# Kernel optimization log

Hardware: AMD Instinct MI355X
Metric: run time of the kernel (lower is better)

Reference implementation:

```python
import jax, jax.numpy as jnp
import numpy as np

B, D_IN, FD = 32768, 2048, 128
N1 = N2 = N3 = 4
T = 1.0  # temperature buffer value (eval mode)
LN_EPS = 1e-5

def _gelu(x):
    return jax.nn.gelu(x, approximate=False)  # torch nn.GELU default = exact erf

def setup_inputs() -> dict:
    key = jax.random.key(0)
    ks = iter(jax.random.split(key, 64))
    def rn(shape, s=0.02):
        return jax.random.normal(next(ks), shape, jnp.float32) * s
    inp = {"x": jax.random.normal(next(ks), (B, D_IN), jnp.float32)}
    # input_proj: Linear(2048,512) GELU Linear(512,256) LayerNorm(256)
    inp.update(ipW1=rn((D_IN, 512)), ipb1=jnp.zeros(512), ipW2=rn((512, 256)), ipb2=jnp.zeros(256),
               ln_g=jnp.ones(256), ln_b=jnp.zeros(256))
    def level(din, nc, pfx):
        return {pfx+"W3d": rn((din, 3)), pfx+"b3d": jnp.zeros(3),
                pfx+"c": rn((nc, 3), 0.3), pfx+"lr": jnp.zeros(nc),
                pfx+"f1W": rn((din, FD)), pfx+"f1b": jnp.zeros(FD),
                pfx+"f2W": rn((FD, FD)), pfx+"f2b": jnp.zeros(FD),
                pfx+"rW": rn((FD+3, nc)), pfx+"rb": jnp.zeros(nc)}
    inp.update(level(256, N1, "l1"))
    inp.update(level(FD, N2, "l2"))
    inp.update(level(FD, N3, "l3"))
    # expert_head: Linear(128+4+4+4, 256) GELU Linear(256, 64)
    inp.update(ehW1=rn((FD+N1+N2+N3, 256)), ehb1=jnp.zeros(256),
               ehW2=rn((256, N1*N2*N3)), ehb2=jnp.zeros(N1*N2*N3))
    return inp

def _level_fwd(x, W3d, b3d, c, f1W, f1b, f2W, f2b, rW, rb):
    # x: (B, din) -> probs (B, nc), features (B, FD)
    pos = x @ W3d + b3d                                   # (B, 3)
    d_sq = ((pos[:, None, :] - c[None, :, :]) ** 2).sum(-1)  # (B, nc)
    geo = -d_sq / (2.0 * T * T + 1e-8)                    # non-spectral geo signal
    feat = _gelu(x @ f1W + f1b) @ f2W + f2b               # (B, FD)
    logits = jnp.concatenate([feat, pos], axis=-1) @ rW + rb + 0.5 * geo
    probs = jax.nn.softmax(logits / max(T, 0.1), axis=-1)  # eval path: plain softmax
    return probs, feat

def _router_fwd(x, ipW1, ipb1, ipW2, ipb2, ln_g, ln_b,
                l1W3d, l1b3d, l1c, l1f1W, l1f1b, l1f2W, l1f2b, l1rW, l1rb,
                l2W3d, l2b3d, l2c, l2f1W, l2f1b, l2f2W, l2f2b, l2rW, l2rb,
                l3W3d, l3b3d, l3c, l3f1W, l3f1b, l3f2W, l3f2b, l3rW, l3rb,
                ehW1, ehb1, ehW2, ehb2):
    h = _gelu(x @ ipW1 + ipb1) @ ipW2 + ipb2
    mu = h.mean(-1, keepdims=True)
    var = ((h - mu) ** 2).mean(-1, keepdims=True)
    h = (h - mu) * jax.lax.rsqrt(var + LN_EPS) * ln_g + ln_b  # LayerNorm(256)
    p1, f1 = _level_fwd(h,  l1W3d, l1b3d, l1c, l1f1W, l1f1b, l1f2W, l1f2b, l1rW, l1rb)
    p2, f2 = _level_fwd(f1, l2W3d, l2b3d, l2c, l2f1W, l2f1b, l2f2W, l2f2b, l2rW, l2rb)
    p3, f3 = _level_fwd(f2, l3W3d, l3b3d, l3c, l3f1W, l3f1b, l3f2W, l3f2b, l3rW, l3rb)
    combined = jnp.concatenate([f3, p1, p2, p3], axis=-1)  # (B, 140)
    logits = _gelu(combined @ ehW1 + ehb1) @ ehW2 + ehb2   # (B, 64)
    expert_probs = jax.nn.softmax(logits / max(T, 0.1), axis=-1)
    return expert_probs

def reference(x, ipW1, ipb1, ipW2, ipb2, ln_g, ln_b,
              l1W3d, l1b3d, l1c, l1lr, l1f1W, l1f1b, l1f2W, l1f2b, l1rW, l1rb,
              l2W3d, l2b3d, l2c, l2lr, l2f1W, l2f1b, l2f2W, l2f2b, l2rW, l2rb,
              l3W3d, l3b3d, l3c, l3lr, l3f1W, l3f1b, l3f2W, l3f2b, l3rW, l3rb,
              ehW1, ehb1, ehW2, ehb2):
    # l?lr (log_radii) are unused in non-spectral mode, matching the source.
    expert_probs = _router_fwd(x, ipW1, ipb1, ipW2, ipb2, ln_g, ln_b,
                               l1W3d, l1b3d, l1c, l1f1W, l1f1b, l1f2W, l1f2b, l1rW, l1rb,
                               l2W3d, l2b3d, l2c, l2f1W, l2f1b, l2f2W, l2f2b, l2rW, l2rb,
                               l3W3d, l3b3d, l3c, l3f1W, l3f1b, l3f2W, l3f2b, l3rW, l3rb,
                               ehW1, ehb1, ehW2, ehb2)
    expert_ids = jnp.argmax(expert_probs, axis=-1)
    return expert_probs, expert_ids
```

## Files before the change

### kernel.cpp

```cpp
#include <hip/hip_runtime.h>
#include <hip/hip_bf16.h>
#include <cstdint>
#include <cstddef>


typedef short  s8v  __attribute__((ext_vector_type(8)));
typedef float  f4v  __attribute__((ext_vector_type(4)));
typedef float  f16v __attribute__((ext_vector_type(16)));
typedef unsigned int u32;

#define B_ROWS 32768

__device__ inline short f2bf(float x) {
    __hip_bfloat16 h = __float2bfloat16(x);
    return __builtin_bit_cast(short, h);
}
__device__ inline float bf2f(short s) {
    return __bfloat162float(__builtin_bit_cast(__hip_bfloat16, s));
}
__device__ inline float gelu_f(float x) {
    return 0.5f * x * (1.0f + erff(x * 0.70710678118654752440f));
}
__device__ inline void gload_lds16(const short* g, short* l) {
    __builtin_amdgcn_global_load_lds(
        (const __attribute__((address_space(1))) u32*)g,
        (__attribute__((address_space(3))) u32*)l, 16, 0, 0);
}

__global__ void split_w1_img(const float* __restrict__ W, short* __restrict__ img)
{
    const int idx = blockIdx.x * 256 + threadIdx.x;
    const int p = idx & 7;
    const int n = (idx >> 3) & 511;
    const int t = idx >> 12;
    const int cs = p ^ (n & 7);
    const int plane = cs >> 2, kc = cs & 3;
    const int kbase = t * 32 + kc * 8;
    s8v v8;
    #pragma unroll
    for (int e = 0; e < 8; ++e) {
        const float v = W[(size_t)(kbase + e) * 512 + n];
        const short h = f2bf(v);
        v8[e] = plane ? f2bf(v - bf2f(h)) : h;
    }
    *(s8v*)&img[(size_t)((t * 512 + n) * 64 + p * 8)] = v8;
}

__launch_bounds__(256, 3)
__global__ void gemm1k(const float* __restrict__ X,
                       const short* __restrict__ Bimg,
                       const float* __restrict__ bias,
                       float* __restrict__ out)
{
    __shared__ short smem[128 * 64 * 3];
    short* Ab  = smem;
    short* Bb0 = smem + 128 * 64;
    short* Bb1 = smem + 128 * 64 * 2;

    const int tid = threadIdx.x;
    const int l = tid & 63, wid = tid >> 6;
    const int wr = wid >> 1, wc = wid & 1;

    const int d = blockIdx.x;
    const int xcd = d & 7, s = d >> 3;
    const int m0 = (xcd * 32 + (s >> 2)) * 128;
    const int n0 = (s & 3) * 128;

    const int ar = tid & 127, ah = tid >> 7;
    const float* xP = X + (size_t)(m0 + ar) * 2048 + ah * 16;
    short* awr = Ab + ar * 64;
    const int pw0 = ((ah * 2    ) ^ (ar & 7)) * 8;
    const int pw1 = ((ah * 2 + 1) ^ (ar & 7)) * 8;
    const int pw2 = ((ah * 2 + 4) ^ (ar & 7)) * 8;
    const int pw3 = ((ah * 2 + 5) ^ (ar & 7)) * 8;

    const short* bP = Bimg + (size_t)n0 * 64 + (size_t)(wid * 4) * 512 + (size_t)l * 8;
    const int bdo = wid * 4 * 512;

    f16v acc[2][2];
    #pragma unroll
    for (int m = 0; m < 2; ++m)
        #pragma unroll
        for (int n = 0; n < 2; ++n) acc[m][n] = (f16v)0.0f;

    f4v cur0, cur1, cur2, cur3;

    auto stageB = [&](int t, short* base) {
        const short* bt = bP + (size_t)t * 32768;
        short* bD = base + bdo;
        gload_lds16(bt,        bD);
        gload_lds16(bt +  512, bD + 512);
        gload_lds16(bt + 1024, bD + 1024);
        gload_lds16(bt + 1536, bD + 1536);
    };
    auto loadA = [&](int t) {
        const float* p = xP + t * 32;
        cur0 = *(const f4v*)(p + 0);
        cur1 = *(const f4v*)(p + 4);
        cur2 = *(const f4v*)(p + 8);
        cur3 = *(const f4v*)(p + 12);
    };
    auto compute = [&](const short* Bb) {
        #pragma unroll
        for (int ks = 0; ks < 2; ++ks) {
            const int ph0 = ks * 2 + (l >> 5);
            s8v ahf[2], alf[2], bhf[2], blf[2];
            #pragma unroll
            for (int m = 0; m < 2; ++m) {
                const int row = wr * 64 + m * 32 + (l & 31);
                const int ph = ph0 ^ (row & 7);
                ahf[m] = *(const s8v*)&Ab[row * 64 + ph * 8];
                alf[m] = *(const s8v*)&Ab[row * 64 + (ph ^ 4) * 8];
            }
            #pragma unroll
            for (int n = 0; n < 2; ++n) {
                const int col = wc * 64 + n * 32 + (l & 31);
                const int ph = ph0 ^ (col & 7);
                bhf[n] = *(const s8v*)&Bb[col * 64 + ph * 8];
                blf[n] = *(const s8v*)&Bb[col * 64 + (ph ^ 4) * 8];
            }
            __builtin_amdgcn_s_setprio(1);
            #pragma unroll
            for (int m = 0; m < 2; ++m)
                #pragma unroll
                for (int n = 0; n < 2; ++n) {
                    acc[m][n] = __builtin_amdgcn_mfma_f32_32x32x16_bf16(ahf[m], bhf[n], acc[m][n], 0, 0, 0);
                    acc[m][n] = __builtin_amdgcn_mfma_f32_32x32x16_bf16(ahf[m], blf[n], acc[m][n], 0, 0, 0);
                    acc[m][n] = __builtin_amdgcn_mfma_f32_32x32x16_bf16(alf[m], bhf[n], acc[m][n], 0, 0, 0);
                }
            __builtin_amdgcn_s_setprio(0);
        }
    };
    auto step = [&](int t, short* bcur, short* bnext) {
        s8v hi0, hi1, lo0, lo1;
        #pragma unroll
        for (int e = 0; e < 4; ++e) {
            float v; short h;
            v = cur0[e]; h = f2bf(v); hi0[e]     = h; lo0[e]     = f2bf(v - bf2f(h));
            v = cur1[e]; h = f2bf(v); hi0[e + 4] = h; lo0[e + 4] = f2bf(v - bf2f(h));
            v = cur2[e]; h = f2bf(v); hi1[e]     = h; lo1[e]     = f2bf(v - bf2f(h));
            v = cur3[e]; h = f2bf(v); hi1[e + 4] = h; lo1[e + 4] = f2bf(v - bf2f(h));
        }
        __builtin_amdgcn_s_barrier();
        __builtin_amdgcn_sched_barrier(0);
        *(s8v*)&awr[pw0] = hi0;
        *(s8v*)&awr[pw1] = hi1;
        *(s8v*)&awr[pw2] = lo0;
        *(s8v*)&awr[pw3] = lo1;
        if (t < 63) {
            stageB(t + 1, bnext);
            __builtin_amdgcn_sched_barrier(0);
            loadA(t + 1);
        }
        asm volatile("s_waitcnt lgkmcnt(0)" ::: "memory");
        __builtin_amdgcn_s_barrier();
        __builtin_amdgcn_sched_barrier(0);
        compute(bcur);
    };

    stageB(0, Bb0);
    __builtin_amdgcn_sched_barrier(0);
    loadA(0);
    for (int t = 0; t < 64; t += 2) {
        step(t,     Bb0, Bb1);
        step(t + 1, Bb1, Bb0);
    }

    #pragma unroll
    for (int m = 0; m < 2; ++m) {
        #pragma unroll
        for (int n = 0; n < 2; ++n) {
            const int gcol = n0 + wc * 64 + n * 32 + (l & 31);
            const float bv = bias[gcol];
            #pragma unroll
            for (int r = 0; r < 16; ++r) {
                const int grow = m0 + wr * 64 + m * 32
                               + (r & 3) + 8 * (r >> 2) + 4 * (l >> 5);
                out[(size_t)grow * 512 + gcol] = gelu_f(acc[m][n][r] + bv);
            }
        }
    }
}

struct SplitDesc { const float* W; short* dst; int K, N, Kpad, blk0; };
struct SplitPack { SplitDesc d[9]; };

__global__ void split_all(SplitPack p) {
    const int bid = blockIdx.x;
    int i = 0;
    #pragma unroll
    for (int j = 1; j < 9; ++j) if (bid >= p.d[j].blk0) i = j;
    const SplitDesc& D = p.d[i];
    const int idx = (bid - D.blk0) * 256 + threadIdx.x;
    const int total = D.N * D.Kpad;
    if (idx >= total) return;
    const int n = idx / D.Kpad, k = idx - n * D.Kpad;
    const float v = (k < D.K) ? D.W[(size_t)k * D.N + n] : 0.0f;
    const short hs = f2bf(v);
    D.dst[idx] = hs;
    D.dst[total + idx] = f2bf(v - bf2f(hs));
}

template<int BM, int BN, int EPI>
__launch_bounds__(256, 2)
__global__ void gemm32(const float* __restrict__ A, int lda,
                       const short* __restrict__ Bsp, int ldb, int NK,
                       const float* __restrict__ bias, int K, int N, int ntiles,
                       int ostr, float* __restrict__ out, float* __restrict__ out2)
{
    constexpr int MF  = BM / 64;
    constexpr int NFw = BN / 64;
    constexpr int BUF = (BM + BN) * 64;
    constexpr int FPT = BM / 8;
    constexpr int TPR = 32 / FPT;
    constexpr int nBI = BN / 32;
    __shared__ short smem[2 * BUF];

    const int tid = threadIdx.x;
    const int l   = tid & 63, wid = tid >> 6;
    const int wr  = wid >> 1, wc = wid & 1;
    const int bid = blockIdx.x;
    const int ntb = bid % ntiles, mtb = bid / ntiles;
    const int m0  = mtb * BM, n0 = ntb * BN;

    const int ar = tid / TPR, aseg = tid % TPR;
    const float* aP = A + (size_t)(m0 + ar) * lda + aseg * FPT;

    const short* bg[nBI];
    {
        const int cs = (l & 7) ^ (l >> 3);
        const int plane = cs >> 2, kslot = cs & 3;
        #pragma unroll
        for (int j = 0; j < nBI; ++j) {
            const int col = (wid * nBI + j) * 8 + (l >> 3);
            bg[j] = Bsp + (size_t)plane * NK + (size_t)(n0 + col) * ldb + kslot * 8;
        }
    }

    f16v acc[MF][NFw];
    #pragma unroll
    for (int m = 0; m < MF; ++m)
        #pragma unroll
        for (int n = 0; n < NFw; ++n) acc[m][n] = (f16v)0.0f;

    f4v areg[FPT / 4];

    auto loadA = [&](int t) {
        const float* p = aP + t * 32;
        #pragma unroll
        for (int i = 0; i < FPT / 4; ++i) areg[i] = *(const f4v*)(p + i * 4);
    };
    auto stageB = [&](int t, short* buf) {
        short* Bb = buf + BM * 64;
        #pragma unroll
        for (int j = 0; j < nBI; ++j)
            gload_lds16(bg[j] + t * 32, Bb + (wid * nBI + j) * 512);
    };
    auto writeA = [&](short* buf) {
        #pragma unroll
        for (int c = 0; c < FPT / 8; ++c) {
            s8v hi, lo;
            #pragma unroll
            for (int e = 0; e < 8; ++e) {
                const float v = areg[c * 2 + (e >> 2)][e & 3];
                const short hs = f2bf(v);
                hi[e] = hs; lo[e] = f2bf(v - bf2f(hs));
            }
            const int csh = aseg * (FPT / 8) + c;
            *(s8v*)&buf[ar * 64 + ((csh    ) ^ (ar & 7)) * 8] = hi;
            *(s8v*)&buf[ar * 64 + ((csh + 4) ^ (ar & 7)) * 8] = lo;
        }
    };
    auto compute = [&](const short* buf) {
        const short* Ab = buf;
        const short* Bb = buf + BM * 64;
        #pragma unroll
        for (int ks = 0; ks < 2; ++ks) {
            const int csb = ks * 2 + (l >> 5);
            s8v ah[MF], al[MF], bh[NFw], bl[NFw];
            #pragma unroll
            for (int m = 0; m < MF; ++m) {
                const int row = wr * (BM / 2) + m * 32 + (l & 31);
                ah[m] = *(const s8v*)&Ab[row * 64 + ((csb    ) ^ (row & 7)) * 8];
                al[m] = *(const s8v*)&Ab[row * 64 + ((csb + 4) ^ (row & 7)) * 8];
            }
            #pragma unroll
            for (int n = 0; n < NFw; ++n) {
                const int col = wc * (BN / 2) + n * 32 + (l & 31);
                bh[n] = *(const s8v*)&Bb[col * 64 + ((csb    ) ^ (col & 7)) * 8];
                bl[n] = *(const s8v*)&Bb[col * 64 + ((csb + 4) ^ (col & 7)) * 8];
            }
            __builtin_amdgcn_s_setprio(1);
            #pragma unroll
            for (int m = 0; m < MF; ++m)
                #pragma unroll
                for (int n = 0; n < NFw; ++n) {
                    acc[m][n] = __builtin_amdgcn_mfma_f32_32x32x16_bf16(ah[m], bh[n], acc[m][n], 0, 0, 0);
                    acc[m][n] = __builtin_amdgcn_mfma_f32_32x32x16_bf16(ah[m], bl[n], acc[m][n], 0, 0, 0);
                    acc[m][n] = __builtin_amdgcn_mfma_f32_32x32x16_bf16(al[m], bh[n], acc[m][n], 0, 0, 0);
                }
            __builtin_amdgcn_s_setprio(0);
        }
    };

    const int NT = K / 32;
    loadA(0);
    stageB(0, smem);
    writeA(smem);
    __syncthreads();
    for (int t = 0; t < NT; ++t) {
        short* curb = smem + (t & 1) * BUF;
        short* nxtb = smem + ((t & 1) ^ 1) * BUF;
        const bool pf = (t + 1 < NT);
        if (pf) { loadA(t + 1); stageB(t + 1, nxtb); }
        compute(curb);
        if (pf) writeA(nxtb);
        __syncthreads();
    }

    if constexpr (EPI <= 1) {
        #pragma unroll
        for (int m = 0; m < MF; ++m) {
            #pragma unroll
            for (int n = 0; n < NFw; ++n) {
                const int gcol = n0 + wc * (BN / 2) + n * 32 + (l & 31);
                const float bv = bias[gcol];
                #pragma unroll
                for (int r = 0; r < 16; ++r) {
                    const int grow = m0 + wr * (BM / 2) + m * 32
                                   + (r & 3) + 8 * (r >> 2) + 4 * (l >> 5);
                    float xv = acc[m][n][r] + bv;
                    if constexpr (EPI == 0) xv = gelu_f(xv);
                    out[(size_t)grow * ostr + gcol] = xv;
                }
            }
        }
    } else {
        float* LT = reinterpret_cast<float*>(smem);
        const int gcolL = wc * 32 + (l & 31);
        const float bv = bias[gcolL];
        #pragma unroll
        for (int r = 0; r < 16; ++r) {
            const int row = wr * 32 + (r & 3) + 8 * (r >> 2) + 4 * (l >> 5);
            LT[row * 64 + gcolL] = acc[0][0][r] + bv;
        }
        __syncthreads();
        const int r = tid >> 2, q = tid & 3;
        const float* Lr = LT + r * 64 + q * 16;
        float mx = Lr[0];
        #pragma unroll
        for (int c = 1; c < 16; ++c) mx = fmaxf(mx, Lr[c]);
        mx = fmaxf(mx, __shfl_xor(mx, 1));
        mx = fmaxf(mx, __shfl_xor(mx, 2));
        float ev[16]; float s = 0.0f;
        #pragma unroll
        for (int c = 0; c < 16; ++c) { ev[c] = expf(Lr[c] - mx); s += ev[c]; }
        s += __shfl_xor(s, 1);
        s += __shfl_xor(s, 2);
        float pmax = -1.0f; int arg = 0;
        #pragma unroll
        for (int c = 0; c < 16; ++c) {
            const float pv = ev[c] / s;
            out[(size_t)(m0 + r) * 64 + q * 16 + c] = pv;
            if (pv > pmax) { pmax = pv; arg = q * 16 + c; }
        }
        #pragma unroll
        for (int off = 1; off <= 2; off <<= 1) {
            const float po = __shfl_xor(pmax, off);
            const int   ao = __shfl_xor(arg, off);
            if (po > pmax || (po == pmax && ao < arg)) { pmax = po; arg = ao; }
        }
        if (q == 0) out2[m0 + r] = (float)arg;
    }
}

__global__ __launch_bounds__(256) void ln_kernel(float* __restrict__ H,
                                                 const float* __restrict__ G,
                                                 const float* __restrict__ Bv)
{
    const int row = blockIdx.x * 4 + (threadIdx.x >> 6);
    const int l   = threadIdx.x & 63;
    float* hr = H + (size_t)row * 256;
    f4v v = *reinterpret_cast<const f4v*>(&hr[l * 4]);
    float s = v[0] + v[1] + v[2] + v[3];
    #pragma unroll
    for (int o = 32; o; o >>= 1) s += __shfl_xor(s, o);
    const float mu = s * 0.00390625f;
    f4v d = v - mu;
    float q = d[0]*d[0] + d[1]*d[1] + d[2]*d[2] + d[3]*d[3];
    #pragma unroll
    for (int o = 32; o; o >>= 1) q += __shfl_xor(q, o);
    const float var = q * 0.00390625f;
    const float sc  = 1.0f / sqrtf(var + 1e-5f);
    f4v gg = *reinterpret_cast<const f4v*>(&G[l * 4]);
    f4v bb = *reinterpret_cast<const f4v*>(&Bv[l * 4]);
    f4v o4 = d * sc * gg + bb;
    *reinterpret_cast<f4v*>(&hr[l * 4]) = o4;
}

__device__ void p_head(int row, int l,
                       const float* __restrict__ X, int din,
                       const float* __restrict__ F, int fstr,
                       const float* __restrict__ W3d, const float* __restrict__ b3d,
                       const float* __restrict__ cc,
                       const float* __restrict__ rW, const float* __restrict__ rb,
                       float* __restrict__ dst)
{
    float px0 = 0.f, px1 = 0.f, px2 = 0.f;
    const int per = din >> 6;
    const float* xr = X + (size_t)row * din;
    for (int i = 0; i < per; ++i) {
        const int k = l + (i << 6);
        const float xv = xr[k];
        px0 += xv * W3d[k*3 + 0];
        px1 += xv * W3d[k*3 + 1];
        px2 += xv * W3d[k*3 + 2];
    }
    float g0 = 0.f, g1 = 0.f, g2 = 0.f, g3 = 0.f;
    const float* fr = F + (size_t)row * fstr;
    #pragma unroll
    for (int i = 0; i < 2; ++i) {
        const int k = l + (i << 6);
        const float fv = fr[k];
        g0 += fv * rW[k*4 + 0]; g1 += fv * rW[k*4 + 1];
        g2 += fv * rW[k*4 + 2]; g3 += fv * rW[k*4 + 3];
    }
    #pragma unroll
    for (int o = 32; o; o >>= 1) {
        px0 += __shfl_xor(px0, o); px1 += __shfl_xor(px1, o); px2 += __shfl_xor(px2, o);
        g0  += __shfl_xor(g0, o);  g1  += __shfl_xor(g1, o);
        g2  += __shfl_xor(g2, o);  g3  += __shfl_xor(g3, o);
    }
    if (l == 0) {
        const float pos0 = px0 + b3d[0], pos1 = px1 + b3d[1], pos2 = px2 + b3d[2];
        float lg[4];
        float mx = -1e30f;
        float gg[4] = {g0, g1, g2, g3};
        #pragma unroll
        for (int c = 0; c < 4; ++c) {
            float a = gg[c] + rb[c]
                    + pos0 * rW[512 + c] + pos1 * rW[516 + c] + pos2 * rW[520 + c];
            const float d0 = pos0 - cc[c*3 + 0];
            const float d1 = pos1 - cc[c*3 + 1];
            const float d2 = pos2 - cc[c*3 + 2];
            a += 0.5f * (-(d0*d0 + d1*d1 + d2*d2) / 2.00000001f);
            lg[c] = a;
            mx = fmaxf(mx, a);
        }
        const float e0 = expf(lg[0]-mx), e1 = expf(lg[1]-mx),
                    e2 = expf(lg[2]-mx), e3 = expf(lg[3]-mx);
        const float s = e0 + e1 + e2 + e3;
        dst[0] = e0/s; dst[1] = e1/s; dst[2] = e2/s; dst[3] = e3/s;
    }
}

struct PAllArgs {
    const float* h2; const float* f1; const float* f2; float* comb;
    const float* W3d[3]; const float* b3d[3]; const float* cc[3];
    const float* rW[3];  const float* rb[3];
};

__global__ __launch_bounds__(256) void p_all(PAllArgs A)
{
    const int row = blockIdx.x * 4 + (threadIdx.x >> 6);
    const int l   = threadIdx.x & 63;
    float* cr = A.comb + (size_t)row * 160;
    p_head(row, l, A.h2, 256, A.f1,  128, A.W3d[0], A.b3d[0], A.cc[0], A.rW[0], A.rb[0], cr + 128);
    p_head(row, l, A.f1, 128, A.f2,  128, A.W3d[1], A.b3d[1], A.cc[1], A.rW[1], A.rb[1], cr + 132);
    p_head(row, l, A.f2, 128, A.comb, 160, A.W3d[2], A.b3d[2], A.cc[2], A.rW[2], A.rb[2], cr + 136);
}

extern "C" void kernel_launch(void* const* d_in, const int* in_sizes, int n_in,
                              void* d_out, int out_size, void* d_ws, size_t ws_size,
                              hipStream_t stream)
{
    (void)in_sizes; (void)n_in; (void)out_size; (void)ws_size;

    const float* x    = (const float*)d_in[0];
    const float* ipW1 = (const float*)d_in[1];
    const float* ipb1 = (const float*)d_in[2];
    const float* ipW2 = (const float*)d_in[3];
    const float* ipb2 = (const float*)d_in[4];
    const float* ln_g = (const float*)d_in[5];
    const float* ln_b = (const float*)d_in[6];
    const float* W3d[3] = {(const float*)d_in[7],  (const float*)d_in[17], (const float*)d_in[27]};
    const float* b3d[3] = {(const float*)d_in[8],  (const float*)d_in[18], (const float*)d_in[28]};
    const float* cc[3]  = {(const float*)d_in[9],  (const float*)d_in[19], (const float*)d_in[29]};
    const float* f1W[3] = {(const float*)d_in[11], (const float*)d_in[21], (const float*)d_in[31]};
    const float* f1b[3] = {(const float*)d_in[12], (const float*)d_in[22], (const float*)d_in[32]};
    const float* f2W[3] = {(const float*)d_in[13], (const float*)d_in[23], (const float*)d_in[33]};
    const float* f2b[3] = {(const float*)d_in[14], (const float*)d_in[24], (const float*)d_in[34]};
    const float* rW[3]  = {(const float*)d_in[15], (const float*)d_in[25], (const float*)d_in[35]};
    const float* rb[3]  = {(const float*)d_in[16], (const float*)d_in[26], (const float*)d_in[36]};
    const float* ehW1 = (const float*)d_in[37];
    const float* ehb1 = (const float*)d_in[38];
    const float* ehW2 = (const float*)d_in[39];
    const float* ehb2 = (const float*)d_in[40];

    size_t off = 0;
    auto take = [&](size_t bytes) -> void* {
        void* p = (char*)d_ws + off;
        off += (bytes + 255) & ~(size_t)255;
        return p;
    };
    auto takeW = [&](int N, int Kpad) -> short* {
        return (short*)take((size_t)2 * N * Kpad * 2);
    };
    short* W1img = (short*)take((size_t)64 * 512 * 64 * 2);
    short* W2s = takeW(256, 512);
    short* L1a = takeW(128, 256);
    short* L1b = takeW(128, 128);
    short* L2a = takeW(128, 128);
    short* L2b = takeW(128, 128);
    short* L3a = takeW(128, 128);
    short* L3b = takeW(128, 128);
    short* E1s = takeW(256, 160);
    short* E2s = takeW(64, 256);
    float* h1  = (float*)take((size_t)B_ROWS * 512 * 4);
    float* h2  = (float*)take((size_t)B_ROWS * 256 * 4);
    float* zg  = (float*)take((size_t)B_ROWS * 128 * 4);
    float* f1  = (float*)take((size_t)B_ROWS * 128 * 4);
    float* f2  = (float*)take((size_t)B_ROWS * 128 * 4);
    float* geh = (float*)take((size_t)B_ROWS * 256 * 4);
    float* comb = h1;

    split_w1_img<<<(64 * 512 * 8) / 256, 256, 0, stream>>>(ipW1, W1img);
    SplitPack sp;
    int blk = 0;
    auto desc = [&](int i, const float* W, short* dst, int K, int N, int Kpad) {
        sp.d[i] = {W, dst, K, N, Kpad, blk};
        blk += (N * Kpad + 255) / 256;
    };
    desc(0, ipW2,   W2s,  512, 256,  512);
    desc(1, f1W[0], L1a,  256, 128,  256);
    desc(2, f2W[0], L1b,  128, 128,  128);
    desc(3, f1W[1], L2a,  128, 128,  128);
    desc(4, f2W[1], L2b,  128, 128,  128);
    desc(5, f1W[2], L3a,  128, 128,  128);
    desc(6, f2W[2], L3b,  128, 128,  128);
    desc(7, ehW1,   E1s,  140, 256,  160);
    desc(8, ehW2,   E2s,  256,  64,  256);
    split_all<<<blk, 256, 0, stream>>>(sp);

    const dim3 blkT(256);
    constexpr int MG128 = B_ROWS / 128;
    constexpr int MG64  = B_ROWS / 64;

    gemm1k<<<1024, blkT, 0, stream>>>(x, W1img, ipb1, h1);
    gemm32<128,128,1><<<MG128*2, blkT, 0, stream>>>(h1, 512, W2s, 512, 256*512, ipb2,
                                                    512, 256, 2, 256, h2, nullptr);
    ln_kernel<<<B_ROWS/4, 256, 0, stream>>>(h2, ln_g, ln_b);

    gemm32<64,128,0><<<MG64, blkT, 0, stream>>>(h2, 256, L1a, 256, 128*256, f1b[0], 256, 128, 1, 128, zg, nullptr);
    gemm32<64,128,1><<<MG64, blkT, 0, stream>>>(zg, 128, L1b, 128, 128*128, f2b[0], 128, 128, 1, 128, f1, nullptr);
    gemm32<64,128,0><<<MG64, blkT, 0, stream>>>(f1, 128, L2a, 128, 128*128, f1b[1], 128, 128, 1, 128, zg, nullptr);
    gemm32<64,128,1><<<MG64, blkT, 0, stream>>>(zg, 128, L2b, 128, 128*128, f2b[1], 128, 128, 1, 128, f2, nullptr);
    gemm32<64,128,0><<<MG64, blkT, 0, stream>>>(f2, 128, L3a, 128, 128*128, f1b[2], 128, 128, 1, 128, zg, nullptr);
    gemm32<64,128,1><<<MG64, blkT, 0, stream>>>(zg, 128, L3b, 128, 128*128, f2b[2], 128, 128, 1, 160, comb, nullptr);

    PAllArgs pa;
    pa.h2 = h2; pa.f1 = f1; pa.f2 = f2; pa.comb = comb;
    for (int i = 0; i < 3; ++i) {
        pa.W3d[i] = W3d[i]; pa.b3d[i] = b3d[i]; pa.cc[i] = cc[i];
        pa.rW[i] = rW[i];   pa.rb[i] = rb[i];
    }
    p_all<<<B_ROWS/4, 256, 0, stream>>>(pa);

    gemm32<64,128,0><<<MG64*2, blkT, 0, stream>>>(comb, 160, E1s, 160, 256*160, ehb1,
                                                  160, 256, 2, 256, geh, nullptr);
    gemm32<64,64,2><<<MG64, blkT, 0, stream>>>(geh, 256, E2s, 256, 64*256, ehb2,
                                               256, 64, 1, 64, (float*)d_out,
                                               (float*)d_out + (size_t)B_ROWS * 64);
}
```

Before: 460.2 us.

## Deepen gemm1k pipeline to prefetch two K-tiles ahead with triple B buffers

The first-layer GEMM now prefetches the B tile and the fp32 A registers two iterations ahead instead of one. It uses three LDS B buffers and two alternating register sets for A, and unrolls the loop by six to rotate them. The aim is to hide more global-load latency behind the MFMA work. In exchange, LDS per block grows from 48KB to 64KB and register use rises, so launch bounds drop to 2 blocks per CU, which lowers occupancy.

```diff
diff --git a/kernel.cpp b/kernel.cpp
--- a/kernel.cpp
+++ b/kernel.cpp
@@ -46,16 +46,17 @@
     *(s8v*)&img[(size_t)((t * 512 + n) * 64 + p * 8)] = v8;
 }
 
-__launch_bounds__(256, 3)
+__launch_bounds__(256, 2)
 __global__ void gemm1k(const float* __restrict__ X,
                        const short* __restrict__ Bimg,
                        const float* __restrict__ bias,
                        float* __restrict__ out)
 {
-    __shared__ short smem[128 * 64 * 3];
-    short* Ab  = smem;
-    short* Bb0 = smem + 128 * 64;
-    short* Bb1 = smem + 128 * 64 * 2;
+    __shared__ short smem[128 * 64 * 4];
+    short* Ab = smem;
+    short* Bu0 = smem + 128 * 64;
+    short* Bu1 = smem + 128 * 64 * 2;
+    short* Bu2 = smem + 128 * 64 * 3;
 
     const int tid = threadIdx.x;
     const int l = tid & 63, wid = tid >> 6;
@@ -83,7 +84,7 @@
         #pragma unroll
         for (int n = 0; n < 2; ++n) acc[m][n] = (f16v)0.0f;
 
-    f4v cur0, cur1, cur2, cur3;
+    f4v s0a, s0b, s0c, s0d, s1a, s1b, s1c, s1d;
 
     auto stageB = [&](int t, short* base) {
         const short* bt = bP + (size_t)t * 32768;
@@ -93,12 +94,12 @@
         gload_lds16(bt + 1024, bD + 1024);
         gload_lds16(bt + 1536, bD + 1536);
     };
-    auto loadA = [&](int t) {
+    auto loadAx = [&](int t, f4v& a, f4v& b, f4v& c, f4v& dd) {
         const float* p = xP + t * 32;
-        cur0 = *(const f4v*)(p + 0);
-        cur1 = *(const f4v*)(p + 4);
-        cur2 = *(const f4v*)(p + 8);
-        cur3 = *(const f4v*)(p + 12);
+        a  = *(const f4v*)(p + 0);
+        b  = *(const f4v*)(p + 4);
+        c  = *(const f4v*)(p + 8);
+        dd = *(const f4v*)(p + 12);
     };
     auto compute = [&](const short* Bb) {
         #pragma unroll
@@ -131,15 +132,16 @@
             __builtin_amdgcn_s_setprio(0);
         }
     };
-    auto step = [&](int t, short* bcur, short* bnext) {
+    auto step = [&](int t, short* bcur, short* bstage,
+                    f4v& a, f4v& b, f4v& c, f4v& dd) {
         s8v hi0, hi1, lo0, lo1;
         #pragma unroll
         for (int e = 0; e < 4; ++e) {
             float v; short h;
-            v = cur0[e]; h = f2bf(v); hi0[e]     = h; lo0[e]     = f2bf(v - bf2f(h));
-            v = cur1[e]; h = f2bf(v); hi0[e + 4] = h; lo0[e + 4] = f2bf(v - bf2f(h));
-            v = cur2[e]; h = f2bf(v); hi1[e]     = h; lo1[e]     = f2bf(v - bf2f(h));
-            v = cur3[e]; h = f2bf(v); hi1[e + 4] = h; lo1[e + 4] = f2bf(v - bf2f(h));
+            v = a[e];  h = f2bf(v); hi0[e]     = h; lo0[e]     = f2bf(v - bf2f(h));
+            v = b[e];  h = f2bf(v); hi0[e + 4] = h; lo0[e + 4] = f2bf(v - bf2f(h));
+            v = c[e];  h = f2bf(v); hi1[e]     = h; lo1[e]     = f2bf(v - bf2f(h));
+            v = dd[e]; h = f2bf(v); hi1[e + 4] = h; lo1[e + 4] = f2bf(v - bf2f(h));
         }
         __builtin_amdgcn_s_barrier();
         __builtin_amdgcn_sched_barrier(0);
@@ -147,10 +149,10 @@
         *(s8v*)&awr[pw1] = hi1;
         *(s8v*)&awr[pw2] = lo0;
         *(s8v*)&awr[pw3] = lo1;
-        if (t < 63) {
-            stageB(t + 1, bnext);
+        if (t + 2 < 64) {
+            stageB(t + 2, bstage);
             __builtin_amdgcn_sched_barrier(0);
-            loadA(t + 1);
+            loadAx(t + 2, a, b, c, dd);
         }
         asm volatile("s_waitcnt lgkmcnt(0)" ::: "memory");
         __builtin_amdgcn_s_barrier();
@@ -158,13 +160,24 @@
         compute(bcur);
     };
 
-    stageB(0, Bb0);
+    stageB(0, Bu0);
+    stageB(1, Bu1);
     __builtin_amdgcn_sched_barrier(0);
-    loadA(0);
-    for (int t = 0; t < 64; t += 2) {
-        step(t,     Bb0, Bb1);
-        step(t + 1, Bb1, Bb0);
-    }
+    loadAx(0, s0a, s0b, s0c, s0d);
+    loadAx(1, s1a, s1b, s1c, s1d);
+
+    for (int i = 0; i < 60; i += 6) {
+        step(i + 0, Bu0, Bu2, s0a, s0b, s0c, s0d);
+        step(i + 1, Bu1, Bu0, s1a, s1b, s1c, s1d);
+        step(i + 2, Bu2, Bu1, s0a, s0b, s0c, s0d);
+        step(i + 3, Bu0, Bu2, s1a, s1b, s1c, s1d);
+        step(i + 4, Bu1, Bu0, s0a, s0b, s0c, s0d);
+        step(i + 5, Bu2, Bu1, s1a, s1b, s1c, s1d);
+    }
+    step(60, Bu0, Bu2, s0a, s0b, s0c, s0d);
+    step(61, Bu1, Bu0, s1a, s1b, s1c, s1d);
+    step(62, Bu2, Bu1, s0a, s0b, s0c, s0d);
+    step(63, Bu0, Bu2, s1a, s1b, s1c, s1d);
 
     #pragma unroll
     for (int m = 0; m < 2; ++m) {
```

New measurement: 468.6 us. About the same (+1.8%).
